# Performance work log

Measured on AMD Instinct MI355X. Metric: run time of the kernel, lower is better.

## Reference

```python
import jax, jax.numpy as jnp
import numpy as np

DIM = 512
NUM_GROUPS = 32
NUM_HEADS = 8
EPS = 1e-5


def group_norm(x, gamma, beta):
    # x: (B, C, H, W); normalize over (C//G, H, W) per group
    B, C, H, W = x.shape
    g = x.reshape(B, NUM_GROUPS, -1)
    mean = g.mean(axis=2, keepdims=True)
    var = g.var(axis=2, keepdims=True)
    g = (g - mean) * jax.lax.rsqrt(var + EPS)
    x = g.reshape(B, C, H, W)
    return x * gamma[None, :, None, None] + beta[None, :, None, None]


def setup_inputs() -> dict:
    key = jax.random.key(0)
    ks = jax.random.split(key, 7)
    B, C, H, W = 16, DIM, 32, 32
    x = jax.random.normal(ks[0], (B, C, H, W), dtype=jnp.float32)
    gamma = jnp.ones((C,), dtype=jnp.float32)
    beta = jnp.zeros((C,), dtype=jnp.float32)
    s_in = 1.0 / np.sqrt(C)
    w_qkv = jax.random.normal(ks[1], (3 * C, C), dtype=jnp.float32) * s_in
    b_qkv = jnp.zeros((3 * C,), dtype=jnp.float32)
    w_proj = jax.random.normal(ks[2], (C, C), dtype=jnp.float32) * s_in
    b_proj = jnp.zeros((C,), dtype=jnp.float32)
    return {"x": x, "gamma": gamma, "beta": beta, "w_qkv": w_qkv,
            "b_qkv": b_qkv, "w_proj": w_proj, "b_proj": b_proj}


def reference(x, gamma, beta, w_qkv, b_qkv, w_proj, b_proj):
    B, C, H, W = x.shape
    nh = NUM_HEADS
    c3 = 3 * C // nh          # per-head qkv channels (3 * head_dim)
    dh = C // nh              # head_dim
    scale = C ** (-0.5)       # NOTE: source scales by full dim, not head_dim

    h = group_norm(x, gamma, beta)

    # 1x1 conv qkv projection: (B, 3C, H, W)
    qkv = jnp.einsum('bchw,oc->bohw', h, w_qkv) + b_qkv[None, :, None, None]

    # rearrange 'b (head c) h w -> (b head) (h w) c'
    qkv = qkv.reshape(B, nh, c3, H, W)
    qkv = qkv.transpose(0, 1, 3, 4, 2).reshape(B * nh, H * W, c3)
    q, k, v = jnp.split(qkv, 3, axis=2)   # each (B*nh, HW, dh)

    score = jnp.einsum('bnc,bmc->bnm', q, k * scale)   # (B*nh, HW, HW)
    attn = jax.nn.softmax(score, axis=2)
    out = jnp.einsum('bnm,bmc->bnc', attn, v)          # (B*nh, HW, dh)

    # rearrange '(head b) (h w) c -> b (head c) h w'  (NOTE head-major, as in source)
    out = out.reshape(nh, B, H, W, dh)
    out = out.transpose(1, 0, 4, 2, 3).reshape(B, C, H, W)

    out = jnp.einsum('bchw,oc->bohw', out, w_proj) + b_proj[None, :, None, None]
    return out + x
```

## Files before the change

### kernel.cpp

```cpp
#include <hip/hip_runtime.h>
#include <stdint.h>

typedef __bf16 bf16;
typedef __attribute__((ext_vector_type(4))) float f32x4;
typedef __attribute__((ext_vector_type(8))) __bf16 bf16x8;
typedef __attribute__((ext_vector_type(4))) __bf16 bf16x4;

#define NB 16
#define CH 512
#define HWS 1024
#define NHEAD 8
#define DH 64
#define O3 1536
#define CPQ 136
#define CPF 132

#define PSW(row, col) (((row) << 6) + (((((col) >> 3) ^ ((row) & 7))) << 3) + ((col) & 7))

__device__ __forceinline__ void gload_lds16(const bf16* g, bf16* l) {
    __builtin_amdgcn_global_load_lds(
        (const __attribute__((address_space(1))) unsigned int*)g,
        (__attribute__((address_space(3))) unsigned int*)l,
        16, 0, 0);
}

#if defined(__has_builtin) && __has_builtin(__builtin_amdgcn_exp2f)
__device__ __forceinline__ float fast_exp2(float x) { return __builtin_amdgcn_exp2f(x); }
#else
__device__ __forceinline__ float fast_exp2(float x) { return exp2f(x); }
#endif

__global__ void prep(const float* __restrict__ x, float* __restrict__ stats,
                     const float* __restrict__ wq, const float* __restrict__ wp,
                     bf16* __restrict__ wq_b, bf16* __restrict__ wp_b) {
    int bx = blockIdx.x;
    if (bx < 512) {
        int b = bx >> 5, g = bx & 31;
        const float4* p = (const float4*)(x + ((size_t)(b * CH + g * 16)) * HWS);
        float s = 0.f, ss = 0.f;
        for (int i = threadIdx.x; i < 4096; i += 256) {
            float4 v = p[i];
            s  += v.x + v.y + v.z + v.w;
            ss += v.x*v.x + v.y*v.y + v.z*v.z + v.w*v.w;
        }
        for (int off = 32; off; off >>= 1) {
            s  += __shfl_xor(s,  off, 64);
            ss += __shfl_xor(ss, off, 64);
        }
        __shared__ float red[8];
        int w = threadIdx.x >> 6;
        if ((threadIdx.x & 63) == 0) { red[w*2] = s; red[w*2+1] = ss; }
        __syncthreads();
        if (threadIdx.x == 0) {
            float S  = red[0] + red[2] + red[4] + red[6];
            float SS = red[1] + red[3] + red[5] + red[7];
            float mean = S * (1.f/16384.f);
            float var  = SS * (1.f/16384.f) - mean*mean;
            stats[bx*2]   = mean;
            stats[bx*2+1] = rsqrtf(var + 1e-5f);
        }
    } else {
        int i = (bx - 512) * 256 + threadIdx.x;
        if (i < O3*CH) wq_b[i] = (bf16)wq[i];
        else           wp_b[i - O3*CH] = (bf16)wp[i - O3*CH];
    }
}

__global__ void gn_apply_t(const float* __restrict__ x, const float* __restrict__ stats,
                           const float* __restrict__ gamma, const float* __restrict__ beta,
                           bf16* __restrict__ hT) {
    __shared__ float tile[32][33];
    int bx = blockIdx.x;
    int b = bx >> 9;
    int rem = bx & 511;
    int ct = rem >> 5, nt = rem & 31;
    int tx = threadIdx.x & 31, ty = threadIdx.x >> 5;
    #pragma unroll
    for (int r = 0; r < 4; ++r) {
        int c = ct*32 + ty + r*8;
        int n = nt*32 + tx;
        float v = x[((size_t)(b * CH + c)) * HWS + n];
        int g = c >> 4;
        float mean = stats[(b*32+g)*2], rstd = stats[(b*32+g)*2+1];
        tile[ty + r*8][tx] = (v - mean) * rstd * gamma[c] + beta[c];
    }
    __syncthreads();
    #pragma unroll
    for (int r = 0; r < 4; ++r) {
        int n = nt*32 + ty + r*8;
        int c = ct*32 + tx;
        hT[((size_t)(b * HWS + n)) * CH + c] = (bf16)tile[tx][ty + r*8];
    }
}

__global__ __launch_bounds__(256, 3)
void qkv_gemm(const bf16* __restrict__ W, const bf16* __restrict__ hT,
              const float* __restrict__ bias, bf16* __restrict__ qkv,
              bf16* __restrict__ vT) {
    __shared__ __align__(16) bf16 SMEM[128*CPQ];
    bf16* As = SMEM;
    bf16* Bs = SMEM + 8192;
    int bx = blockIdx.x;
    int po = bx >> 7, qo = bx & 127;
    int obase = po*128, bnbase = qo*128;
    int tid = threadIdx.x;
    int lane = tid & 63, w = tid >> 6;
    int quad = lane >> 4, l15 = lane & 15;
    int wm = w >> 1, wn = w & 1;
    int x7 = l15 & 7;
    int srow = lane >> 3, spos = lane & 7;
    int sgc = (spos ^ srow) * 8;

    f32x4 acc[4][4] = {};
    for (int k0 = 0; k0 < 512; k0 += 64) {
        #pragma unroll
        for (int r = 0; r < 4; ++r) {
            int rb = r*32 + w*8;
            gload_lds16(W  + ((size_t)(obase  + rb + srow))*512 + k0 + sgc, &As[rb*64]);
            gload_lds16(hT + ((size_t)(bnbase + rb + srow))*512 + k0 + sgc, &Bs[rb*64]);
        }
        __syncthreads();
        #pragma unroll
        for (int ks = 0; ks < 2; ++ks) {
            int ch = (ks*4 + quad) ^ x7;
            bf16x8 af[4], bfv[4];
            #pragma unroll
            for (int mt = 0; mt < 4; ++mt)
                af[mt] = *(const bf16x8*)(&As[(wm*64 + mt*16 + l15)*64 + ch*8]);
            #pragma unroll
            for (int nt = 0; nt < 4; ++nt)
                bfv[nt] = *(const bf16x8*)(&Bs[(wn*64 + nt*16 + l15)*64 + ch*8]);
            #pragma unroll
            for (int mt = 0; mt < 4; ++mt)
                #pragma unroll
                for (int nt = 0; nt < 4; ++nt)
                    acc[mt][nt] = __builtin_amdgcn_mfma_f32_16x16x32_bf16(af[mt], bfv[nt], acc[mt][nt], 0, 0, 0);
        }
        __syncthreads();
    }

    bf16* Cs = SMEM;
    int b = bnbase >> 10;
    int nbase = bnbase & 1023;
    #pragma unroll
    for (int mt = 0; mt < 4; ++mt) {
        int o0 = obase + wm*64 + mt*16 + quad*4;
        float4 bb = *(const float4*)(bias + o0);
        int c192 = o0 % 192;
        bool isV = (c192 >= 128);
        int h = o0 / 192;
        int d0 = c192 - 128;
        #pragma unroll
        for (int nt = 0; nt < 4; ++nt) {
            int bn_l = wn*64 + nt*16 + l15;
            bf16x4 v;
            v[0] = (bf16)(acc[mt][nt][0] + bb.x);
            v[1] = (bf16)(acc[mt][nt][1] + bb.y);
            v[2] = (bf16)(acc[mt][nt][2] + bb.z);
            v[3] = (bf16)(acc[mt][nt][3] + bb.w);
            *(bf16x4*)(&Cs[bn_l*CPQ + (o0 - obase)]) = v;
            if (isV) {
                int key = nbase + bn_l;
                size_t vb_ = ((size_t)((b*8 + h)*64 + d0)) * HWS + key;
                vT[vb_]          = v[0];
                vT[vb_ + HWS]    = v[1];
                vT[vb_ + 2*HWS]  = v[2];
                vT[vb_ + 3*HWS]  = v[3];
            }
        }
    }
    __syncthreads();
    #pragma unroll
    for (int p = 0; p < 8; ++p) {
        int bn_l = p*16 + (tid >> 4);
        int o8 = (tid & 15) * 8;
        if ((obase + o8) % 192 < 128) {
            uint4 v = *(const uint4*)(&Cs[bn_l*CPQ + o8]);
            *(uint4*)(qkv + ((size_t)(bnbase + bn_l)) * O3 + obase + o8) = v;
        }
    }
}

__global__ __launch_bounds__(256, 2)
void flash_attn(const bf16* __restrict__ qkv, const bf16* __restrict__ vT,
                bf16* __restrict__ A2) {
    __shared__ __align__(16) bf16 Ks[2][64*64];
    __shared__ __align__(16) bf16 Vs[2][64*64];
    __shared__ __align__(16) bf16 Ps[4][64*64];
    int bx = blockIdx.x;
    int g = bx & 127, qt = bx >> 7;
    int b = g >> 3, h = g & 7;
    int tid = threadIdx.x, lane = tid & 63, w = tid >> 6;
    int quad = lane >> 4, l15 = lane & 15;
    int x7 = l15 & 7;
    int srow = lane >> 3, spos = lane & 7;
    int sgc = (spos ^ srow) * 8;
    const float kLog2 = 0.04419417382415922f * 1.44269504088896341f;

    bf16x8 aq[4][2];
    #pragma unroll
    for (int mt = 0; mt < 4; ++mt) {
        int qrow = qt*256 + w*64 + mt*16 + l15;
        const bf16* qb = qkv + ((size_t)(b * HWS + qrow)) * O3 + h*192;
        aq[mt][0] = *(const bf16x8*)(qb + quad*8);
        aq[mt][1] = *(const bf16x8*)(qb + 32 + quad*8);
        #pragma unroll
        for (int j = 0; j < 8; ++j) {
            aq[mt][0][j] = (bf16)((float)aq[mt][0][j] * kLog2);
            aq[mt][1][j] = (bf16)((float)aq[mt][1][j] * kLog2);
        }
    }

    const bf16* kg = qkv + ((size_t)(b*HWS + w*16 + srow))*O3 + h*192 + 64 + sgc;
    const bf16* vg = vT  + ((size_t)(g*DH  + w*16 + srow))*HWS + sgc;

    gload_lds16(kg,                  &Ks[0][(w*16)*64]);
    gload_lds16(kg + (size_t)8*O3,   &Ks[0][(w*16 + 8)*64]);
    gload_lds16(vg,                  &Vs[0][(w*16)*64]);
    gload_lds16(vg + (size_t)8*HWS,  &Vs[0][(w*16 + 8)*64]);

    f32x4 acc[4][4] = {};
    f32x4 L4[4] = {};
    __syncthreads();

    for (int kt = 0; kt < 16; ++kt) {
        int cur = kt & 1;
        if (kt < 15) {
            gload_lds16(kg + (size_t)((kt+1)*64)*O3,     &Ks[cur^1][(w*16)*64]);
            gload_lds16(kg + (size_t)((kt+1)*64 + 8)*O3, &Ks[cur^1][(w*16 + 8)*64]);
            gload_lds16(vg + (kt+1)*64,                  &Vs[cur^1][(w*16)*64]);
            gload_lds16(vg + (size_t)8*HWS + (kt+1)*64,  &Vs[cur^1][(w*16 + 8)*64]);
        }
        const bf16* Kc = &Ks[cur][0];
        const bf16* Vc = &Vs[cur][0];

        #pragma unroll
        for (int nt = 0; nt < 4; ++nt) {
            bf16x8 ak0 = *(const bf16x8*)(&Kc[(nt*16 + l15)*64 + ((quad     ^ x7)*8)]);
            bf16x8 ak1 = *(const bf16x8*)(&Kc[(nt*16 + l15)*64 + (((quad+4) ^ x7)*8)]);
            #pragma unroll
            for (int mt = 0; mt < 4; ++mt) {
                f32x4 z = {};
                z = __builtin_amdgcn_mfma_f32_16x16x32_bf16(ak0, aq[mt][0], z, 0, 0, 0);
                z = __builtin_amdgcn_mfma_f32_16x16x32_bf16(ak1, aq[mt][1], z, 0, 0, 0);
                bf16x4 p;
                #pragma unroll
                for (int r = 0; r < 4; ++r) {
                    float e = fast_exp2(z[r]);
                    L4[mt][r] += e;
                    p[r] = (bf16)e;
                }
                *(bf16x4*)(&Ps[w][PSW(mt*16 + l15, nt*16 + quad*4)]) = p;
            }
        }
        bf16x8 ap[4][2];
        #pragma unroll
        for (int mt = 0; mt < 4; ++mt) {
            ap[mt][0] = *(const bf16x8*)(&Ps[w][PSW(mt*16 + l15, quad*8)]);
            ap[mt][1] = *(const bf16x8*)(&Ps[w][PSW(mt*16 + l15, 32 + quad*8)]);
        }
        #pragma unroll
        for (int dt = 0; dt < 4; ++dt) {
            bf16x8 bv0 = *(const bf16x8*)(&Vc[(dt*16 + l15)*64 + ((quad     ^ x7)*8)]);
            bf16x8 bv1 = *(const bf16x8*)(&Vc[(dt*16 + l15)*64 + (((quad+4) ^ x7)*8)]);
            #pragma unroll
            for (int mt = 0; mt < 4; ++mt) {
                acc[mt][dt] = __builtin_amdgcn_mfma_f32_16x16x32_bf16(ap[mt][0], bv0, acc[mt][dt], 0, 0, 0);
                acc[mt][dt] = __builtin_amdgcn_mfma_f32_16x16x32_bf16(ap[mt][1], bv1, acc[mt][dt], 0, 0, 0);
            }
        }
        __syncthreads();
    }

    float Linv[4][4];
    #pragma unroll
    for (int mt = 0; mt < 4; ++mt) {
        float Lf = (L4[mt][0] + L4[mt][1]) + (L4[mt][2] + L4[mt][3]);
        Lf += __shfl_xor(Lf, 16, 64);
        Lf += __shfl_xor(Lf, 32, 64);
        #pragma unroll
        for (int r = 0; r < 4; ++r)
            Linv[mt][r] = 1.f / __shfl(Lf, quad*4 + r, 64);
    }

    #pragma unroll
    for (int mt = 0; mt < 4; ++mt)
        #pragma unroll
        for (int dt = 0; dt < 4; ++dt)
            #pragma unroll
            for (int r = 0; r < 4; ++r)
                Ps[w][PSW(mt*16 + quad*4 + r, dt*16 + l15)] = (bf16)(acc[mt][dt][r] * Linv[mt][r]);

    int bp = g & 15;
    int hp = g >> 4;
    #pragma unroll
    for (int cc = 0; cc < 8; ++cc) {
        int c = cc*64 + lane;
        int row = c >> 3, dcc = c & 7;
        uint4 v = *(const uint4*)(&Ps[w][PSW(row, dcc*8)]);
        size_t idx = ((size_t)(bp * HWS + qt*256 + w*64 + row)) * CH + hp*64 + dcc*8;
        *(uint4*)(A2 + idx) = v;
    }
}

__global__ __launch_bounds__(256, 3)
void proj_gemm(const bf16* __restrict__ A2, const bf16* __restrict__ Wp,
               const float* __restrict__ bias, const float* __restrict__ x,
               float* __restrict__ out) {
    __shared__ __align__(16) bf16 SMEM[16896];
    bf16* As = SMEM;
    bf16* Bs = SMEM + 8192;
    int bx = blockIdx.x;
    int po = bx >> 7, qo = bx & 127;
    int obase = po*128, bnbase = qo*128;
    int tid = threadIdx.x;
    int lane = tid & 63, w = tid >> 6;
    int quad = lane >> 4, l15 = lane & 15;
    int wm = w >> 1, wn = w & 1;
    int x7 = l15 & 7;
    int srow = lane >> 3, spos = lane & 7;
    int sgc = (spos ^ srow) * 8;

    f32x4 acc[4][4] = {};
    for (int k0 = 0; k0 < 512; k0 += 64) {
        #pragma unroll
        for (int r = 0; r < 4; ++r) {
            int rb = r*32 + w*8;
            gload_lds16(A2 + ((size_t)(bnbase + rb + srow))*512 + k0 + sgc, &As[rb*64]);
            gload_lds16(Wp + ((size_t)(obase  + rb + srow))*512 + k0 + sgc, &Bs[rb*64]);
        }
        __syncthreads();
        #pragma unroll
        for (int ks = 0; ks < 2; ++ks) {
            int ch = (ks*4 + quad) ^ x7;
            bf16x8 af[4], bfv[4];
            #pragma unroll
            for (int mt = 0; mt < 4; ++mt)
                af[mt] = *(const bf16x8*)(&As[(wm*64 + mt*16 + l15)*64 + ch*8]);
            #pragma unroll
            for (int nt = 0; nt < 4; ++nt)
                bfv[nt] = *(const bf16x8*)(&Bs[(wn*64 + nt*16 + l15)*64 + ch*8]);
            #pragma unroll
            for (int mt = 0; mt < 4; ++mt)
                #pragma unroll
                for (int nt = 0; nt < 4; ++nt)
                    acc[mt][nt] = __builtin_amdgcn_mfma_f32_16x16x32_bf16(af[mt], bfv[nt], acc[mt][nt], 0, 0, 0);
        }
        __syncthreads();
    }

    float* Cf = (float*)SMEM;
    int bb = bnbase >> 10;
    int nbase = bnbase & 1023;
    #pragma unroll
    for (int hh = 0; hh < 2; ++hh) {
        if (wm == hh) {
            #pragma unroll
            for (int mt = 0; mt < 4; ++mt)
                #pragma unroll
                for (int nt = 0; nt < 4; ++nt)
                    #pragma unroll
                    for (int r = 0; r < 4; ++r)
                        Cf[(mt*16 + quad*4 + r)*CPF + wn*64 + nt*16 + l15] = acc[mt][nt][r];
        }
        __syncthreads();
        #pragma unroll
        for (int p = 0; p < 4; ++p) {
            int ol = p*32 + (tid >> 3);
            int nl0 = (tid & 7) * 8;
            int o = obase + ol;
            float bv = bias[o];
            #pragma unroll
            for (int jj = 0; jj < 2; ++jj) {
                int nl = nl0 + jj*4;
                size_t idx = ((size_t)(bb * CH + o)) * HWS + nbase + hh*64 + nl;
                float4 xr = *(const float4*)(x + idx);
                float4 res;
                res.x = Cf[(nl+0)*CPF + ol] + bv + xr.x;
                res.y = Cf[(nl+1)*CPF + ol] + bv + xr.y;
                res.z = Cf[(nl+2)*CPF + ol] + bv + xr.z;
                res.w = Cf[(nl+3)*CPF + ol] + bv + xr.w;
                *(float4*)(out + idx) = res;
            }
        }
        __syncthreads();
    }
}

extern "C" void kernel_launch(void* const* d_in, const int* in_sizes, int n_in,
                              void* d_out, int out_size, void* d_ws, size_t ws_size,
                              hipStream_t stream) {
    const float* x      = (const float*)d_in[0];
    const float* gamma  = (const float*)d_in[1];
    const float* beta   = (const float*)d_in[2];
    const float* w_qkv  = (const float*)d_in[3];
    const float* b_qkv  = (const float*)d_in[4];
    const float* w_proj = (const float*)d_in[5];
    const float* b_proj = (const float*)d_in[6];
    float* out = (float*)d_out;

    char* ws = (char*)d_ws;
    float* stats = (float*)(ws + 0);
    bf16*  wq_b  = (bf16*)(ws + 4096);
    bf16*  wp_b  = (bf16*)(ws + 1576960);
    bf16*  hT    = (bf16*)(ws + 2101248);
    bf16*  qkv   = (bf16*)(ws + 18878464);
    bf16*  vT    = (bf16*)(ws + 69210112);
    bf16*  A2    = hT;

    prep       <<<4608, 256, 0, stream>>>(x, stats, w_qkv, w_proj, wq_b, wp_b);
    gn_apply_t <<<8192, 256, 0, stream>>>(x, stats, gamma, beta, hT);
    qkv_gemm   <<<1536, 256, 0, stream>>>(wq_b, hT, b_qkv, qkv, vT);
    flash_attn <<<512,  256, 0, stream>>>(qkv, vT, A2);
    proj_gemm  <<<512,  256, 0, stream>>>(A2, wp_b, b_proj, x, out);
}
```

Measured before the change: 199.5 us.

## Use 32x32x16 MFMA in flash attention and keep P in registers

```diff
diff --git a/kernel.cpp b/kernel.cpp
--- a/kernel.cpp
+++ b/kernel.cpp
@@ -3,6 +3,8 @@
 
 typedef __bf16 bf16;
 typedef __attribute__((ext_vector_type(4))) float f32x4;
+typedef __attribute__((ext_vector_type(16))) float f32x16;
+typedef __attribute__((ext_vector_type(4))) int i32x4;
 typedef __attribute__((ext_vector_type(8))) __bf16 bf16x8;
 typedef __attribute__((ext_vector_type(4))) __bf16 bf16x4;
 
@@ -14,8 +16,7 @@
 #define O3 1536
 #define CPQ 136
 #define CPF 132
-
-#define PSW(row, col) (((row) << 6) + (((((col) >> 3) ^ ((row) & 7))) << 3) + ((col) & 7))
+#define OPD 72
 
 __device__ __forceinline__ void gload_lds16(const bf16* g, bf16* l) {
     __builtin_amdgcn_global_load_lds(
@@ -29,6 +30,12 @@
 #else
 __device__ __forceinline__ float fast_exp2(float x) { return exp2f(x); }
 #endif
+
+__device__ __forceinline__ unsigned int pkbf(float a, float b) {
+    unsigned short lo = __builtin_bit_cast(unsigned short, (bf16)a);
+    unsigned short hi = __builtin_bit_cast(unsigned short, (bf16)b);
+    return (unsigned int)lo | ((unsigned int)hi << 16);
+}
 
 __global__ void prep(const float* __restrict__ x, float* __restrict__ stats,
                      const float* __restrict__ wq, const float* __restrict__ wp,
@@ -181,33 +188,33 @@
     }
 }
 
-__global__ __launch_bounds__(256, 2)
+__global__ __launch_bounds__(256, 3)
 void flash_attn(const bf16* __restrict__ qkv, const bf16* __restrict__ vT,
                 bf16* __restrict__ A2) {
     __shared__ __align__(16) bf16 Ks[2][64*64];
     __shared__ __align__(16) bf16 Vs[2][64*64];
-    __shared__ __align__(16) bf16 Ps[4][64*64];
+    __shared__ __align__(16) bf16 Ps[4][32*OPD];
     int bx = blockIdx.x;
     int g = bx & 127, qt = bx >> 7;
     int b = g >> 3, h = g & 7;
     int tid = threadIdx.x, lane = tid & 63, w = tid >> 6;
-    int quad = lane >> 4, l15 = lane & 15;
-    int x7 = l15 & 7;
+    int l31 = lane & 31, hi = lane >> 5;
+    bool hib = (hi != 0);
+    int x7l = l31 & 7;
     int srow = lane >> 3, spos = lane & 7;
     int sgc = (spos ^ srow) * 8;
     const float kLog2 = 0.04419417382415922f * 1.44269504088896341f;
 
-    bf16x8 aq[4][2];
-    #pragma unroll
-    for (int mt = 0; mt < 4; ++mt) {
-        int qrow = qt*256 + w*64 + mt*16 + l15;
-        const bf16* qb = qkv + ((size_t)(b * HWS + qrow)) * O3 + h*192;
-        aq[mt][0] = *(const bf16x8*)(qb + quad*8);
-        aq[mt][1] = *(const bf16x8*)(qb + 32 + quad*8);
-        #pragma unroll
-        for (int j = 0; j < 8; ++j) {
-            aq[mt][0][j] = (bf16)((float)aq[mt][0][j] * kLog2);
-            aq[mt][1][j] = (bf16)((float)aq[mt][1][j] * kLog2);
+    bf16x8 aq[4];
+    {
+        int qrow = qt*128 + w*32 + l31;
+        const bf16* qb = qkv + ((size_t)(b * HWS + qrow)) * O3 + h*192 + hi*8;
+        #pragma unroll
+        for (int seg = 0; seg < 4; ++seg) {
+            aq[seg] = *(const bf16x8*)(qb + seg*16);
+            #pragma unroll
+            for (int j = 0; j < 8; ++j)
+                aq[seg][j] = (bf16)((float)aq[seg][j] * kLog2);
         }
     }
 
@@ -219,8 +226,8 @@
     gload_lds16(vg,                  &Vs[0][(w*16)*64]);
     gload_lds16(vg + (size_t)8*HWS,  &Vs[0][(w*16 + 8)*64]);
 
-    f32x4 acc[4][4] = {};
-    f32x4 L4[4] = {};
+    f32x16 acc[2] = {};
+    f32x4 L4 = {};
     __syncthreads();
 
     for (int kt = 0; kt < 16; ++kt) {
@@ -234,72 +241,79 @@
         const bf16* Kc = &Ks[cur][0];
         const bf16* Vc = &Vs[cur][0];
 
-        #pragma unroll
-        for (int nt = 0; nt < 4; ++nt) {
-            bf16x8 ak0 = *(const bf16x8*)(&Kc[(nt*16 + l15)*64 + ((quad     ^ x7)*8)]);
-            bf16x8 ak1 = *(const bf16x8*)(&Kc[(nt*16 + l15)*64 + (((quad+4) ^ x7)*8)]);
-            #pragma unroll
-            for (int mt = 0; mt < 4; ++mt) {
-                f32x4 z = {};
-                z = __builtin_amdgcn_mfma_f32_16x16x32_bf16(ak0, aq[mt][0], z, 0, 0, 0);
-                z = __builtin_amdgcn_mfma_f32_16x16x32_bf16(ak1, aq[mt][1], z, 0, 0, 0);
-                bf16x4 p;
-                #pragma unroll
-                for (int r = 0; r < 4; ++r) {
-                    float e = fast_exp2(z[r]);
-                    L4[mt][r] += e;
-                    p[r] = (bf16)e;
-                }
-                *(bf16x4*)(&Ps[w][PSW(mt*16 + l15, nt*16 + quad*4)]) = p;
+        bf16x8 pa[4];
+        #pragma unroll
+        for (int kb = 0; kb < 2; ++kb) {
+            f32x16 z = {};
+            #pragma unroll
+            for (int seg = 0; seg < 4; ++seg) {
+                bf16x8 ak = *(const bf16x8*)(&Kc[(kb*32 + l31)*64 + (((seg*2 + hi) ^ x7l)*8)]);
+                z = __builtin_amdgcn_mfma_f32_32x32x16_bf16(ak, aq[seg], z, 0, 0, 0);
             }
-        }
-        bf16x8 ap[4][2];
-        #pragma unroll
-        for (int mt = 0; mt < 4; ++mt) {
-            ap[mt][0] = *(const bf16x8*)(&Ps[w][PSW(mt*16 + l15, quad*8)]);
-            ap[mt][1] = *(const bf16x8*)(&Ps[w][PSW(mt*16 + l15, 32 + quad*8)]);
-        }
-        #pragma unroll
-        for (int dt = 0; dt < 4; ++dt) {
-            bf16x8 bv0 = *(const bf16x8*)(&Vc[(dt*16 + l15)*64 + ((quad     ^ x7)*8)]);
-            bf16x8 bv1 = *(const bf16x8*)(&Vc[(dt*16 + l15)*64 + (((quad+4) ^ x7)*8)]);
-            #pragma unroll
-            for (int mt = 0; mt < 4; ++mt) {
-                acc[mt][dt] = __builtin_amdgcn_mfma_f32_16x16x32_bf16(ap[mt][0], bv0, acc[mt][dt], 0, 0, 0);
-                acc[mt][dt] = __builtin_amdgcn_mfma_f32_16x16x32_bf16(ap[mt][1], bv1, acc[mt][dt], 0, 0, 0);
+            float e[16];
+            #pragma unroll
+            for (int r = 0; r < 16; ++r) {
+                e[r] = fast_exp2(z[r]);
+                L4[r & 3] += e[r];
             }
-        }
-        __syncthreads();
-    }
-
-    float Linv[4][4];
-    #pragma unroll
-    for (int mt = 0; mt < 4; ++mt) {
-        float Lf = (L4[mt][0] + L4[mt][1]) + (L4[mt][2] + L4[mt][3]);
-        Lf += __shfl_xor(Lf, 16, 64);
-        Lf += __shfl_xor(Lf, 32, 64);
-        #pragma unroll
-        for (int r = 0; r < 4; ++r)
-            Linv[mt][r] = 1.f / __shfl(Lf, quad*4 + r, 64);
-    }
-
-    #pragma unroll
-    for (int mt = 0; mt < 4; ++mt)
-        #pragma unroll
-        for (int dt = 0; dt < 4; ++dt)
-            #pragma unroll
-            for (int r = 0; r < 4; ++r)
-                Ps[w][PSW(mt*16 + quad*4 + r, dt*16 + l15)] = (bf16)(acc[mt][dt][r] * Linv[mt][r]);
+            unsigned int w8[8];
+            #pragma unroll
+            for (int i = 0; i < 8; ++i)
+                w8[i] = pkbf(e[2*i], e[2*i + 1]);
+            unsigned int p0 = __shfl_xor((int)w8[0], 32, 64);
+            unsigned int p1 = __shfl_xor((int)w8[1], 32, 64);
+            unsigned int p2 = __shfl_xor((int)w8[2], 32, 64);
+            unsigned int p3 = __shfl_xor((int)w8[3], 32, 64);
+            unsigned int p4 = __shfl_xor((int)w8[4], 32, 64);
+            unsigned int p5 = __shfl_xor((int)w8[5], 32, 64);
+            unsigned int p6 = __shfl_xor((int)w8[6], 32, 64);
+            unsigned int p7 = __shfl_xor((int)w8[7], 32, 64);
+            i32x4 f0, f1;
+            f0[0] = (int)(hib ? p2 : w8[0]);
+            f0[1] = (int)(hib ? p3 : w8[1]);
+            f0[2] = (int)(hib ? w8[2] : p0);
+            f0[3] = (int)(hib ? w8[3] : p1);
+            f1[0] = (int)(hib ? p6 : w8[4]);
+            f1[1] = (int)(hib ? p7 : w8[5]);
+            f1[2] = (int)(hib ? w8[6] : p4);
+            f1[3] = (int)(hib ? w8[7] : p5);
+            pa[kb*2 + 0] = __builtin_bit_cast(bf16x8, f0);
+            pa[kb*2 + 1] = __builtin_bit_cast(bf16x8, f1);
+        }
+
+        #pragma unroll
+        for (int db = 0; db < 2; ++db)
+            #pragma unroll
+            for (int ks = 0; ks < 4; ++ks) {
+                bf16x8 av = *(const bf16x8*)(&Vc[(db*32 + l31)*64 + (((ks*2 + hi) ^ x7l)*8)]);
+                acc[db] = __builtin_amdgcn_mfma_f32_32x32x16_bf16(av, pa[ks], acc[db], 0, 0, 0);
+            }
+        __syncthreads();
+    }
+
+    float Lf = (L4[0] + L4[1]) + (L4[2] + L4[3]);
+    Lf += __shfl_xor(Lf, 32, 64);
+    float Linv = 1.f / Lf;
+
+    bf16* Psw = &Ps[w][0];
+    #pragma unroll
+    for (int db = 0; db < 2; ++db)
+        #pragma unroll
+        for (int i = 0; i < 8; ++i) {
+            int d = db*32 + (i >> 1)*8 + (i & 1)*2 + 4*hi;
+            unsigned int wv = pkbf(acc[db][2*i] * Linv, acc[db][2*i + 1] * Linv);
+            *(unsigned int*)(&Psw[l31*OPD + d]) = wv;
+        }
 
     int bp = g & 15;
     int hp = g >> 4;
     #pragma unroll
-    for (int cc = 0; cc < 8; ++cc) {
-        int c = cc*64 + lane;
-        int row = c >> 3, dcc = c & 7;
-        uint4 v = *(const uint4*)(&Ps[w][PSW(row, dcc*8)]);
-        size_t idx = ((size_t)(bp * HWS + qt*256 + w*64 + row)) * CH + hp*64 + dcc*8;
-        *(uint4*)(A2 + idx) = v;
+    for (int cc = 0; cc < 4; ++cc) {
+        int idx = cc*64 + lane;
+        int q = idx >> 3, dcc = idx & 7;
+        uint4 v = *(const uint4*)(&Psw[q*OPD + dcc*8]);
+        size_t oidx = ((size_t)(bp * HWS + qt*128 + w*32 + q)) * CH + hp*64 + dcc*8;
+        *(uint4*)(A2 + oidx) = v;
     }
 }
 
@@ -411,6 +425,6 @@
     prep       <<<4608, 256, 0, stream>>>(x, stats, w_qkv, w_proj, wq_b, wp_b);
     gn_apply_t <<<8192, 256, 0, stream>>>(x, stats, gamma, beta, hT);
     qkv_gemm   <<<1536, 256, 0, stream>>>(wq_b, hT, b_qkv, qkv, vT);
-    flash_attn <<<512,  256, 0, stream>>>(qkv, vT, A2);
+    flash_attn <<<1024, 256, 0, stream>>>(qkv, vT, A2);
     proj_gemm  <<<512,  256, 0, stream>>>(A2, wp_b, b_proj, x, out);
 }
```

Result: slower. 220.6 us (+10.6%).
